# Kernel tuning notes

Hardware: AMD Instinct MI355X
Metric: run time of the kernel (lower is better)

The kernel has to match this reference:

```python
import jax, jax.numpy as jnp
import numpy as np

D = 1024
H = 16
HD = D // H  # 64


def setup_inputs() -> dict:
    key = jax.random.key(0)
    ks = jax.random.split(key, 11)
    B, L = 2, 2048
    std = 0.02
    return {
        "query": jax.random.normal(ks[0], (B, L, D), jnp.float32),
        "key": jax.random.normal(ks[1], (B, L, D), jnp.float32),
        "value": jax.random.normal(ks[2], (B, L, D), jnp.float32),
        "Wq": jax.random.normal(ks[3], (D, D), jnp.float32) * std,
        "bq": jnp.zeros((D,), jnp.float32),
        "Wk": jax.random.normal(ks[4], (D, D), jnp.float32) * std,
        "bk": jnp.zeros((D,), jnp.float32),
        "Wv": jax.random.normal(ks[5], (D, D), jnp.float32) * std,
        "bv": jnp.zeros((D,), jnp.float32),
        "Wo": jax.random.normal(ks[6], (D, D), jnp.float32) * std,
        "bo": jnp.zeros((D,), jnp.float32),
    }


def _split_heads(x):
    # [B, L, D] -> [B, H, L, HD]
    B, L, _ = x.shape
    return x.reshape(B, L, H, HD).transpose(0, 2, 1, 3)


def reference(query, key, value, Wq, bq, Wk, bk, Wv, bv, Wo, bo):
    B, Lq, _ = query.shape
    # Linear projections (torch Linear: x @ W.T + b)
    Q = _split_heads(query @ Wq.T + bq)
    K = _split_heads(key @ Wk.T + bk)
    V = _split_heads(value @ Wv.T + bv)
    scale = HD ** -0.5
    scores = jnp.einsum("bhqd,bhkd->bhqk", Q, K) * scale  # [B,H,Lq,Lk]
    weights = jax.nn.softmax(scores, axis=-1)
    attended = jnp.einsum("bhqk,bhkd->bhqd", weights, V)  # [B,H,Lq,HD]
    attended = attended.transpose(0, 2, 1, 3).reshape(B, Lq, D)
    output = attended @ Wo.T + bo
    return output, weights.mean(axis=1)
```

## Files before the change

### kernel.cpp

```cpp
#include <hip/hip_runtime.h>
#include <stdint.h>

#define D_MODEL 1024
#define NHEAD 16
#define HDIM 64
#define SEQ 2048
#define NTOK 4096
#define KVB 128
#define NT (KVB / 16)

typedef unsigned short u16;
typedef float f32x4 __attribute__((ext_vector_type(4)));
typedef __bf16 bf16x8 __attribute__((ext_vector_type(8)));
typedef unsigned int u32x4 __attribute__((ext_vector_type(4)));
typedef u16 u16x4 __attribute__((ext_vector_type(4)));

#define QSC 0.180336880111117f

__device__ __forceinline__ u16 fcast_bf(float f) {
  __bf16 h = (__bf16)f;
  return __builtin_bit_cast(u16, h);
}

__device__ __forceinline__ float exp2_fast(float x) {
#if __has_builtin(__builtin_amdgcn_exp2f)
  return __builtin_amdgcn_exp2f(x);
#else
  return __expf(x * 0.69314718056f);
#endif
}

__device__ __forceinline__ bf16x8 scale_q(bf16x8 q) {
  bf16x8 r;
#pragma unroll
  for (int i = 0; i < 8; i++) r[i] = (__bf16)((float)q[i] * QSC);
  return r;
}

__device__ __forceinline__ bf16x8 lds_frag(const u16* sm, int off) {
  return *reinterpret_cast<const bf16x8*>(sm + off);
}

__device__ __forceinline__ void gload_lds16(const u16* g, u16* l) {
  __builtin_amdgcn_global_load_lds((const __attribute__((address_space(1))) void*)g,
                                   (__attribute__((address_space(3))) void*)l, 16, 0, 0);
}

__global__ void cvt3_kernel(const float* __restrict__ s0, const float* __restrict__ s1,
                            const float* __restrict__ s2, u16* __restrict__ dst, int n4) {
  const float* s = blockIdx.y == 0 ? s0 : (blockIdx.y == 1 ? s1 : s2);
  u16* d = dst + (size_t)blockIdx.y * n4 * 4;
  int i = blockIdx.x * blockDim.x + threadIdx.x;
  int stride = gridDim.x * blockDim.x;
  for (; i < n4; i += stride) {
    f32x4 v = reinterpret_cast<const f32x4*>(s)[i];
    u16x4 o;
    o[0] = fcast_bf(v[0]); o[1] = fcast_bf(v[1]);
    o[2] = fcast_bf(v[2]); o[3] = fcast_bf(v[3]);
    reinterpret_cast<u16x4*>(d)[i] = o;
  }
}

__global__ void cvt4_kernel(const float* __restrict__ s0, const float* __restrict__ s1,
                            const float* __restrict__ s2, const float* __restrict__ s3,
                            u16* __restrict__ dst, int n4) {
  const float* s = blockIdx.y == 0 ? s0 : (blockIdx.y == 1 ? s1 : (blockIdx.y == 2 ? s2 : s3));
  u16* d = dst + (size_t)blockIdx.y * n4 * 4;
  int i = blockIdx.x * blockDim.x + threadIdx.x;
  int stride = gridDim.x * blockDim.x;
  for (; i < n4; i += stride) {
    f32x4 v = reinterpret_cast<const f32x4*>(s)[i];
    u16x4 o;
    o[0] = fcast_bf(v[0]); o[1] = fcast_bf(v[1]);
    o[2] = fcast_bf(v[2]); o[3] = fcast_bf(v[3]);
    reinterpret_cast<u16x4*>(d)[i] = o;
  }
}

template<int MODE>
__global__ __launch_bounds__(256)
void gemm_kernel(const u16* __restrict__ Abase, const u16* __restrict__ Wbase,
                 const float* __restrict__ b0, const float* __restrict__ b1,
                 const float* __restrict__ b2,
                 u16* __restrict__ obf, float* __restrict__ of32) {
  const int z = (MODE == 0) ? blockIdx.z : 0;
  const u16* A = Abase + (size_t)z * NTOK * D_MODEL;
  const u16* W = Wbase + (size_t)z * D_MODEL * D_MODEL;
  const float* bias = (MODE == 0) ? (z == 0 ? b0 : (z == 1 ? b1 : b2)) : b0;
  u16* oz = (MODE == 0) ? (obf + (size_t)z * NTOK * D_MODEL) : obf;

  const int flat = blockIdx.y * 8 + blockIdx.x;
  const int nf = (flat & 7) * 32 + (flat >> 3);
  const int bn0 = (nf & 7) * 128;
  const int bm0 = (nf >> 3) * 128;
  const int tid = threadIdx.x;
  const int lane = tid & 63, wid = tid >> 6;
  const int wm = wid >> 1, wn = wid & 1;
  const int l15 = lane & 15, l4 = lane >> 4;
  const int lrow8 = lane >> 3, lch = lane & 7;

  __shared__ u16 smA[128 * 64];
  __shared__ u16 smB[128 * 64];

  f32x4 acc[4][4];
#pragma unroll
  for (int mi = 0; mi < 4; mi++)
#pragma unroll
    for (int ni = 0; ni < 4; ni++) acc[mi][ni] = f32x4{0.f, 0.f, 0.f, 0.f};

  for (int it = 0; it < D_MODEL / 64; it++) {
    const int k0 = it * 64;
    __syncthreads();
#pragma unroll
    for (int c2 = 0; c2 < 4; c2++) {
      int blk = wid * 4 + c2;
      int base16 = blk * 512;
      int row = blk * 8 + lrow8;
      gload_lds16(A + (size_t)(bm0 + row) * D_MODEL + k0 + lch * 8, &smA[base16]);
      gload_lds16(W + (size_t)(bn0 + row) * D_MODEL + k0 + lch * 8, &smB[base16]);
    }
    __syncthreads();
#pragma unroll
    for (int kk = 0; kk < 2; kk++) {
      bf16x8 af[4], bfv[4];
#pragma unroll
      for (int mi = 0; mi < 4; mi++) {
        int r = wm * 64 + mi * 16 + l15;
        af[mi] = lds_frag(smA, r * 64 + (kk * 4 + l4) * 8);
      }
#pragma unroll
      for (int ni = 0; ni < 4; ni++) {
        int r = wn * 64 + ni * 16 + l15;
        bfv[ni] = lds_frag(smB, r * 64 + (kk * 4 + l4) * 8);
      }
#pragma unroll
      for (int mi = 0; mi < 4; mi++)
#pragma unroll
        for (int ni = 0; ni < 4; ni++)
          acc[mi][ni] = __builtin_amdgcn_mfma_f32_16x16x32_bf16(af[mi], bfv[ni], acc[mi][ni], 0, 0, 0);
    }
  }

#pragma unroll
  for (int mi = 0; mi < 4; mi++) {
#pragma unroll
    for (int ni = 0; ni < 4; ni++) {
      int colg = bn0 + wn * 64 + ni * 16 + l15;
      float bv = bias[colg];
      if (MODE == 0 && z == 2) {
        int h = colg >> 6, hd = colg & 63;
        int row0 = bm0 + wm * 64 + mi * 16 + l4 * 4;
        int b = row0 >> 11, lq = row0 & 2047;
        u16x4 pk;
#pragma unroll
        for (int j = 0; j < 4; j++) pk[j] = fcast_bf(acc[mi][ni][j] + bv);
        size_t idx = ((size_t)((b * NHEAD + h) * HDIM + hd)) * SEQ + lq;
        *reinterpret_cast<u16x4*>(oz + idx) = pk;
      } else {
#pragma unroll
        for (int j = 0; j < 4; j++) {
          int rowg = bm0 + wm * 64 + mi * 16 + l4 * 4 + j;
          float v = acc[mi][ni][j] + bv;
          if (MODE == 0) {
            int b = rowg >> 11, lq = rowg & 2047;
            int h = colg >> 6, hd = colg & 63;
            oz[((size_t)((b * NHEAD + h) * SEQ + lq)) * HDIM + hd] = fcast_bf(v);
          } else {
            of32[(size_t)rowg * D_MODEL + colg] = v;
          }
        }
      }
    }
  }
}

__global__ __launch_bounds__(512)
void attn_kernel(const u16* __restrict__ Qh, const u16* __restrict__ Kh,
                 const u16* __restrict__ Vh, u16* __restrict__ attb,
                 float* __restrict__ m_ws, float* __restrict__ linv_ws) {
  const int qt0 = blockIdx.x * 128;
  const int bh = blockIdx.y;
  const int b = bh >> 4, h = bh & 15;
  const int tid = threadIdx.x;
  const int lane = tid & 63, wid = tid >> 6;
  const int l15 = lane & 15, l4 = lane >> 4;

  const u16* Qp = Qh + (size_t)bh * SEQ * HDIM;
  const u16* Kp = Kh + (size_t)bh * SEQ * HDIM;
  const u16* Vp = Vh + (size_t)bh * HDIM * SEQ;

  __shared__ u16 smK[KVB * 64];
  __shared__ u16 smV[64 * KVB];
  __shared__ u16 smP[8][16 * KVB];

  bf16x8 qf[2];
  {
    const u16* qrow = Qp + (size_t)(qt0 + wid * 16 + l15) * HDIM;
    qf[0] = scale_q(*reinterpret_cast<const bf16x8*>(qrow + l4 * 8));
    qf[1] = scale_q(*reinterpret_cast<const bf16x8*>(qrow + 32 + l4 * 8));
  }

  float m = -1e30f, lsum = 0.f;
  f32x4 oacc[4];
#pragma unroll
  for (int d = 0; d < 4; d++) oacc[d] = f32x4{0.f, 0.f, 0.f, 0.f};

  u32x4 rk[2], rv[2];
#pragma unroll
  for (int i = 0; i < 2; i++) {
    int c = i * 512 + tid;
    rk[i] = *reinterpret_cast<const u32x4*>(Kp + (size_t)(c >> 3) * HDIM + (c & 7) * 8);
    rv[i] = *reinterpret_cast<const u32x4*>(Vp + (size_t)(c >> 4) * SEQ + (c & 15) * 8);
  }

  for (int kt = 0; kt < SEQ / KVB; kt++) {
    __syncthreads();
#pragma unroll
    for (int i = 0; i < 2; i++) {
      int c = i * 512 + tid;
      { int row = c >> 3, ch = c & 7;
        *reinterpret_cast<u32x4*>(&smK[row * 64 + ((ch ^ (row & 7)) * 8)]) = rk[i]; }
      { int row = c >> 4, ch = c & 15;
        *reinterpret_cast<u32x4*>(&smV[row * KVB + ((ch ^ (row & 15)) * 8)]) = rv[i]; }
    }
    __syncthreads();
    if (kt + 1 < SEQ / KVB) {
      int kn = (kt + 1) * KVB;
#pragma unroll
      for (int i = 0; i < 2; i++) {
        int c = i * 512 + tid;
        rk[i] = *reinterpret_cast<const u32x4*>(Kp + (size_t)(kn + (c >> 3)) * HDIM + (c & 7) * 8);
        rv[i] = *reinterpret_cast<const u32x4*>(Vp + (size_t)(c >> 4) * SEQ + kn + (c & 15) * 8);
      }
    }
    f32x4 s[NT];
#pragma unroll
    for (int nt = 0; nt < NT; nt++) s[nt] = f32x4{0.f, 0.f, 0.f, 0.f};
#pragma unroll
    for (int kk = 0; kk < 2; kk++) {
#pragma unroll
      for (int nt = 0; nt < NT; nt++) {
        int r = nt * 16 + l15;
        int ch = (kk * 4 + l4) ^ (r & 7);
        bf16x8 kf = lds_frag(smK, r * 64 + ch * 8);
        s[nt] = __builtin_amdgcn_mfma_f32_16x16x32_bf16(kf, qf[kk], s[nt], 0, 0, 0);
      }
    }
    float smax = s[0][0];
#pragma unroll
    for (int nt = 0; nt < NT; nt++)
#pragma unroll
      for (int j = 0; j < 4; j++) smax = fmaxf(smax, s[nt][j]);
    smax = fmaxf(smax, __shfl_xor(smax, 16));
    smax = fmaxf(smax, __shfl_xor(smax, 32));
    float mn = fmaxf(m, smax);
    float corr = exp2_fast(m - mn);
    m = mn;
    float ps = 0.f;
#pragma unroll
    for (int nt = 0; nt < NT; nt++) {
      u16x4 pwv;
#pragma unroll
      for (int j = 0; j < 4; j++) {
        float pv = exp2_fast(s[nt][j] - mn);
        ps += pv;
        pwv[j] = fcast_bf(pv);
      }
      int sp = (nt * 4 + l4) ^ (l15 * 2);
      *reinterpret_cast<u16x4*>(&smP[wid][l15 * KVB + sp * 4]) = pwv;
    }
    ps += __shfl_xor(ps, 16);
    ps += __shfl_xor(ps, 32);
    lsum = lsum * corr + ps;
#pragma unroll
    for (int d = 0; d < 4; d++)
#pragma unroll
      for (int j = 0; j < 4; j++) oacc[d][j] *= corr;
#pragma unroll
    for (int kc = 0; kc < 4; kc++) {
      int chp = (kc * 4 + l4) ^ l15;
      bf16x8 pf = lds_frag(smP[wid], l15 * KVB + chp * 8);
#pragma unroll
      for (int d = 0; d < 4; d++) {
        int r = d * 16 + l15;
        int ch = (kc * 4 + l4) ^ (r & 15);
        bf16x8 vf = lds_frag(smV, r * KVB + ch * 8);
        oacc[d] = __builtin_amdgcn_mfma_f32_16x16x32_bf16(vf, pf, oacc[d], 0, 0, 0);
      }
    }
  }

  const float li = 1.f / lsum;
  const int token = qt0 + wid * 16 + l15;
  if (l4 == 0) {
    m_ws[(size_t)bh * SEQ + token] = m;
    linv_ws[(size_t)bh * SEQ + token] = li;
  }
#pragma unroll
  for (int d = 0; d < 4; d++) {
    u16x4 pk;
#pragma unroll
    for (int j = 0; j < 4; j++) pk[j] = fcast_bf(oacc[d][j] * li);
    *reinterpret_cast<u16x4*>(
        attb + ((size_t)(b * SEQ + token)) * D_MODEL + h * HDIM + d * 16 + l4 * 4) = pk;
  }
}

__global__ __launch_bounds__(512)
void mean_kernel(const u16* __restrict__ Qh, const u16* __restrict__ Kh,
                 const float* __restrict__ m_ws, const float* __restrict__ linv_ws,
                 float* __restrict__ out1) {
  const int kt0 = blockIdx.x * 64;
  const int qt0 = blockIdx.y * 128;
  const int b = blockIdx.z;
  const int tid = threadIdx.x;
  const int lane = tid & 63, wid = tid >> 6;
  const int l15 = lane & 15, l4 = lane >> 4;

  __shared__ u16 smK[2][64 * 64];

  f32x4 macc[4];
#pragma unroll
  for (int nt = 0; nt < 4; nt++) macc[nt] = f32x4{0.f, 0.f, 0.f, 0.f};

  const int rbase = qt0 + wid * 16 + l4 * 4;
  const size_t qoff = (size_t)(qt0 + wid * 16 + l15) * HDIM;
  const int srow = tid >> 3, sch = tid & 7;
  const int soff = srow * 64 + ((sch ^ (srow & 7)) * 8);

  u32x4 rk;
  bf16x8 qfa, qfb;
  {
    const u16* Kp0 = Kh + (size_t)(b * NHEAD) * SEQ * HDIM;
    rk = *reinterpret_cast<const u32x4*>(Kp0 + (size_t)(kt0 + srow) * HDIM + sch * 8);
    const u16* Qp0 = Qh + (size_t)(b * NHEAD) * SEQ * HDIM + qoff;
    qfa = scale_q(*reinterpret_cast<const bf16x8*>(Qp0 + l4 * 8));
    qfb = scale_q(*reinterpret_cast<const bf16x8*>(Qp0 + 32 + l4 * 8));
  }

  for (int h = 0; h < NHEAD; h++) {
    const int bh = b * NHEAD + h;
    u16* kbuf = &smK[h & 1][0];
    *reinterpret_cast<u32x4*>(&kbuf[soff]) = rk;
    __syncthreads();
    u32x4 rkn;
    bf16x8 qfan, qfbn;
    if (h + 1 < NHEAD) {
      const u16* Kp1 = Kh + (size_t)(bh + 1) * SEQ * HDIM;
      rkn = *reinterpret_cast<const u32x4*>(Kp1 + (size_t)(kt0 + srow) * HDIM + sch * 8);
      const u16* Qp1 = Qh + (size_t)(bh + 1) * SEQ * HDIM + qoff;
      qfan = scale_q(*reinterpret_cast<const bf16x8*>(Qp1 + l4 * 8));
      qfbn = scale_q(*reinterpret_cast<const bf16x8*>(Qp1 + 32 + l4 * 8));
    }
    f32x4 s[4];
#pragma unroll
    for (int nt = 0; nt < 4; nt++) s[nt] = f32x4{0.f, 0.f, 0.f, 0.f};
#pragma unroll
    for (int kk = 0; kk < 2; kk++) {
#pragma unroll
      for (int nt = 0; nt < 4; nt++) {
        int r = nt * 16 + l15;
        int ch = (kk * 4 + l4) ^ (r & 7);
        bf16x8 kf = lds_frag(kbuf, r * 64 + ch * 8);
        s[nt] = __builtin_amdgcn_mfma_f32_16x16x32_bf16(kk == 0 ? qfa : qfb, kf, s[nt], 0, 0, 0);
      }
    }
    f32x4 mv = *reinterpret_cast<const f32x4*>(&m_ws[(size_t)bh * SEQ + rbase]);
    f32x4 lv = *reinterpret_cast<const f32x4*>(&linv_ws[(size_t)bh * SEQ + rbase]);
#pragma unroll
    for (int nt = 0; nt < 4; nt++)
#pragma unroll
      for (int j = 0; j < 4; j++)
        macc[nt][j] += exp2_fast(s[nt][j] - mv[j]) * lv[j];
    if (h + 1 < NHEAD) {
      rk = rkn;
      qfa = qfan; qfb = qfbn;
    }
  }
  const float invh = 1.f / 16.f;
#pragma unroll
  for (int nt = 0; nt < 4; nt++)
#pragma unroll
    for (int j = 0; j < 4; j++)
      out1[((size_t)(b * SEQ + rbase + j)) * SEQ + kt0 + nt * 16 + l15] = macc[nt][j] * invh;
}

extern "C" void kernel_launch(void* const* d_in, const int* in_sizes, int n_in,
                              void* d_out, int out_size, void* d_ws, size_t ws_size,
                              hipStream_t stream) {
  (void)in_sizes; (void)n_in; (void)out_size; (void)ws_size;
  const float* query = (const float*)d_in[0];
  const float* key = (const float*)d_in[1];
  const float* value = (const float*)d_in[2];
  const float* Wq = (const float*)d_in[3];
  const float* bq = (const float*)d_in[4];
  const float* Wk = (const float*)d_in[5];
  const float* bk = (const float*)d_in[6];
  const float* Wv = (const float*)d_in[7];
  const float* bv = (const float*)d_in[8];
  const float* Wo = (const float*)d_in[9];
  const float* bo = (const float*)d_in[10];

  char* ws = (char*)d_ws;
  u16* xb = (u16*)(ws);
  u16* wb = (u16*)(ws + 25165824);
  u16* Qhp = (u16*)(ws + 33554432);
  u16* attb = (u16*)(ws + 58720256);
  float* m_ws = (float*)(ws + 67108864);
  float* linv_ws = (float*)(ws + 67371008);

  float* out0 = (float*)d_out;
  float* out1 = out0 + (size_t)NTOK * D_MODEL;

  cvt3_kernel<<<dim3(512, 3), 256, 0, stream>>>(query, key, value, xb, 1048576);
  cvt4_kernel<<<dim3(192, 4), 256, 0, stream>>>(Wq, Wk, Wv, Wo, wb, 262144);

  gemm_kernel<0><<<dim3(8, 32, 3), 256, 0, stream>>>(xb, wb, bq, bk, bv, Qhp, nullptr);
  attn_kernel<<<dim3(16, 32), 512, 0, stream>>>(Qhp, Qhp + 4194304, Qhp + 8388608,
                                                attb, m_ws, linv_ws);
  mean_kernel<<<dim3(32, 16, 2), 512, 0, stream>>>(Qhp, Qhp + 4194304, m_ws, linv_ws, out1);
  gemm_kernel<1><<<dim3(8, 32, 1), 256, 0, stream>>>(attb, wb + 3 * 1048576, bo, bo, bo,
                                                     nullptr, out0);
}
```

Measured before the change: 205.5 us.

## Load K fragments directly to registers in mean kernel, drop LDS staging

```diff
diff --git a/kernel.cpp b/kernel.cpp
--- a/kernel.cpp
+++ b/kernel.cpp
@@ -306,75 +306,67 @@
   }
 }
 
-__global__ __launch_bounds__(512)
+__global__ __launch_bounds__(256)
 void mean_kernel(const u16* __restrict__ Qh, const u16* __restrict__ Kh,
                  const float* __restrict__ m_ws, const float* __restrict__ linv_ws,
                  float* __restrict__ out1) {
   const int kt0 = blockIdx.x * 64;
-  const int qt0 = blockIdx.y * 128;
+  const int qt0 = blockIdx.y * 64;
   const int b = blockIdx.z;
   const int tid = threadIdx.x;
   const int lane = tid & 63, wid = tid >> 6;
   const int l15 = lane & 15, l4 = lane >> 4;
 
-  __shared__ u16 smK[2][64 * 64];
+  const int rbase = qt0 + wid * 16 + l4 * 4;
+  const size_t hstride = (size_t)SEQ * HDIM;
+  const u16* Kp = Kh + (size_t)(b * NHEAD) * hstride + (size_t)(kt0 + l15) * HDIM + l4 * 8;
+  const u16* Qp = Qh + (size_t)(b * NHEAD) * hstride + (size_t)(qt0 + wid * 16 + l15) * HDIM + l4 * 8;
+  const float* mp = m_ws + (size_t)(b * NHEAD) * SEQ + rbase;
+  const float* lp = linv_ws + (size_t)(b * NHEAD) * SEQ + rbase;
 
   f32x4 macc[4];
 #pragma unroll
   for (int nt = 0; nt < 4; nt++) macc[nt] = f32x4{0.f, 0.f, 0.f, 0.f};
 
-  const int rbase = qt0 + wid * 16 + l4 * 4;
-  const size_t qoff = (size_t)(qt0 + wid * 16 + l15) * HDIM;
-  const int srow = tid >> 3, sch = tid & 7;
-  const int soff = srow * 64 + ((sch ^ (srow & 7)) * 8);
-
-  u32x4 rk;
-  bf16x8 qfa, qfb;
-  {
-    const u16* Kp0 = Kh + (size_t)(b * NHEAD) * SEQ * HDIM;
-    rk = *reinterpret_cast<const u32x4*>(Kp0 + (size_t)(kt0 + srow) * HDIM + sch * 8);
-    const u16* Qp0 = Qh + (size_t)(b * NHEAD) * SEQ * HDIM + qoff;
-    qfa = scale_q(*reinterpret_cast<const bf16x8*>(Qp0 + l4 * 8));
-    qfb = scale_q(*reinterpret_cast<const bf16x8*>(Qp0 + 32 + l4 * 8));
-  }
-
+  bf16x8 kf[8], qa, qb;
+#pragma unroll
+  for (int f = 0; f < 8; f++)
+    kf[f] = *reinterpret_cast<const bf16x8*>(Kp + (size_t)(f & 3) * 16 * HDIM + (f >> 2) * 32);
+  qa = *reinterpret_cast<const bf16x8*>(Qp);
+  qb = *reinterpret_cast<const bf16x8*>(Qp + 32);
+
+#pragma unroll
   for (int h = 0; h < NHEAD; h++) {
-    const int bh = b * NHEAD + h;
-    u16* kbuf = &smK[h & 1][0];
-    *reinterpret_cast<u32x4*>(&kbuf[soff]) = rk;
-    __syncthreads();
-    u32x4 rkn;
-    bf16x8 qfan, qfbn;
+    bf16x8 kn[8], qan, qbn;
     if (h + 1 < NHEAD) {
-      const u16* Kp1 = Kh + (size_t)(bh + 1) * SEQ * HDIM;
-      rkn = *reinterpret_cast<const u32x4*>(Kp1 + (size_t)(kt0 + srow) * HDIM + sch * 8);
-      const u16* Qp1 = Qh + (size_t)(bh + 1) * SEQ * HDIM + qoff;
-      qfan = scale_q(*reinterpret_cast<const bf16x8*>(Qp1 + l4 * 8));
-      qfbn = scale_q(*reinterpret_cast<const bf16x8*>(Qp1 + 32 + l4 * 8));
-    }
+      const u16* Kn = Kp + (size_t)(h + 1) * hstride;
+      const u16* Qn = Qp + (size_t)(h + 1) * hstride;
+#pragma unroll
+      for (int f = 0; f < 8; f++)
+        kn[f] = *reinterpret_cast<const bf16x8*>(Kn + (size_t)(f & 3) * 16 * HDIM + (f >> 2) * 32);
+      qan = *reinterpret_cast<const bf16x8*>(Qn);
+      qbn = *reinterpret_cast<const bf16x8*>(Qn + 32);
+    }
+    bf16x8 qas = scale_q(qa), qbs = scale_q(qb);
     f32x4 s[4];
 #pragma unroll
     for (int nt = 0; nt < 4; nt++) s[nt] = f32x4{0.f, 0.f, 0.f, 0.f};
 #pragma unroll
-    for (int kk = 0; kk < 2; kk++) {
-#pragma unroll
-      for (int nt = 0; nt < 4; nt++) {
-        int r = nt * 16 + l15;
-        int ch = (kk * 4 + l4) ^ (r & 7);
-        bf16x8 kf = lds_frag(kbuf, r * 64 + ch * 8);
-        s[nt] = __builtin_amdgcn_mfma_f32_16x16x32_bf16(kk == 0 ? qfa : qfb, kf, s[nt], 0, 0, 0);
-      }
-    }
-    f32x4 mv = *reinterpret_cast<const f32x4*>(&m_ws[(size_t)bh * SEQ + rbase]);
-    f32x4 lv = *reinterpret_cast<const f32x4*>(&linv_ws[(size_t)bh * SEQ + rbase]);
+    for (int kk = 0; kk < 2; kk++)
+#pragma unroll
+      for (int nt = 0; nt < 4; nt++)
+        s[nt] = __builtin_amdgcn_mfma_f32_16x16x32_bf16(kk ? qbs : qas, kf[kk * 4 + nt], s[nt], 0, 0, 0);
+    f32x4 mv = *reinterpret_cast<const f32x4*>(mp + (size_t)h * SEQ);
+    f32x4 lv = *reinterpret_cast<const f32x4*>(lp + (size_t)h * SEQ);
 #pragma unroll
     for (int nt = 0; nt < 4; nt++)
 #pragma unroll
       for (int j = 0; j < 4; j++)
         macc[nt][j] += exp2_fast(s[nt][j] - mv[j]) * lv[j];
     if (h + 1 < NHEAD) {
-      rk = rkn;
-      qfa = qfan; qfb = qfbn;
+#pragma unroll
+      for (int f = 0; f < 8; f++) kf[f] = kn[f];
+      qa = qan; qb = qbn;
     }
   }
   const float invh = 1.f / 16.f;
@@ -418,7 +410,7 @@
   gemm_kernel<0><<<dim3(8, 32, 3), 256, 0, stream>>>(xb, wb, bq, bk, bv, Qhp, nullptr);
   attn_kernel<<<dim3(16, 32), 512, 0, stream>>>(Qhp, Qhp + 4194304, Qhp + 8388608,
                                                 attb, m_ws, linv_ws);
-  mean_kernel<<<dim3(32, 16, 2), 512, 0, stream>>>(Qhp, Qhp + 4194304, m_ws, linv_ws, out1);
+  mean_kernel<<<dim3(32, 32, 2), 256, 0, stream>>>(Qhp, Qhp + 4194304, m_ws, linv_ws, out1);
   gemm_kernel<1><<<dim3(8, 32, 1), 256, 0, stream>>>(attb, wb + 3 * 1048576, bo, bo, bo,
                                                      nullptr, out0);
 }
```

New measurement: 310.8 us. 51.3% more time.
